# Optimization experiments

Measured on AMD Instinct MI355X. Metric: run time of the kernel, lower is better.

The kernel has to match this reference:

```python
import jax, jax.numpy as jnp
import numpy as np

B, C_IN, T = 32, 22, 5000
EMB, P = 64, 100
HOP, NFFT, SR = 25, 128, 250
MIN_SZ, MAX_SZ = 10, 100
OC = 40
SCALES = (9, 25, 49)
FC = OC * len(SCALES)
_freqs = np.arange(NFFT // 2 + 1) * SR / NFFT
MU_IDX = np.nonzero((_freqs >= 8) & (_freqs <= 13))[0]   # bins 5,6
BETA_IDX = np.nonzero((_freqs >= 13) & (_freqs <= 30))[0]  # bins 7..15


def setup_inputs() -> dict:
    key = jax.random.key(0)
    k = iter(jax.random.split(key, 16))
    inp = {"x": jax.random.normal(next(k), (B, C_IN, T), jnp.float32)}
    for i, s in enumerate(SCALES):
        inp[f"ms{i}_w1"] = jax.random.normal(next(k), (OC, 1, 1, s), jnp.float32) * 0.05
        inp[f"ms{i}_b1"] = jnp.zeros((OC,), jnp.float32)
        inp[f"ms{i}_w2"] = jax.random.normal(next(k), (OC, OC, C_IN, 1), jnp.float32) * 0.05
        inp[f"ms{i}_b2"] = jnp.zeros((OC,), jnp.float32)
        inp[f"ms{i}_g"] = jnp.ones((OC,), jnp.float32)
        inp[f"ms{i}_bt"] = jnp.zeros((OC,), jnp.float32)
        inp[f"ms{i}_m"] = jnp.zeros((OC,), jnp.float32)
        inp[f"ms{i}_v"] = jnp.ones((OC,), jnp.float32)
    inp["a_w1"] = jax.random.normal(next(k), (C_IN // 2, C_IN, 3), jnp.float32) * 0.05
    inp["a_b1"] = jnp.zeros((C_IN // 2,), jnp.float32)
    inp["a_g"] = jnp.ones((C_IN // 2,), jnp.float32)
    inp["a_bt"] = jnp.zeros((C_IN // 2,), jnp.float32)
    inp["a_m"] = jnp.zeros((C_IN // 2,), jnp.float32)
    inp["a_v"] = jnp.ones((C_IN // 2,), jnp.float32)
    inp["a_w2"] = jax.random.normal(next(k), (1, C_IN // 2, 1), jnp.float32) * 0.05
    inp["a_b2"] = jnp.zeros((1,), jnp.float32)
    inp["proj_w"] = jax.random.normal(next(k), (EMB, FC, 1), jnp.float32) * 0.05
    inp["proj_b"] = jnp.zeros((EMB,), jnp.float32)
    return inp


def _conv1d(x, w, pad):
    return jax.lax.conv_general_dilated(x, w, (1,), [(pad, pad)],
                                        dimension_numbers=("NCH", "OIH", "NCH"))


def _bn(y, g, bt, m, v):  # eval-mode BatchNorm over channel dim of [B, C, T]
    return (y - m[None, :, None]) * jax.lax.rsqrt(v[None, :, None] + 1e-5) * g[None, :, None] + bt[None, :, None]


def _branch(x, w1, b1, w2, b2, g, bt, m, v):
    # Conv2d(1,OC,(1,ks)) on [B,1,C,T] == per-channel 1D conv over time.
    oc, _, _, ks = w1.shape
    b_, c_, t_ = x.shape
    y = _conv1d(x.reshape(b_ * c_, 1, t_), w1.reshape(oc, 1, ks), (ks - 1) // 2) + b1[None, :, None]
    y = y.reshape(b_, c_, oc, t_).transpose(0, 2, 1, 3)            # [B, OC, C, T]
    # Conv2d(OC,OC,(C,1)) collapses the channel (height) dim.
    y = jnp.einsum("oih,biht->bot", w2[..., 0], y) + b2[None, :, None]
    return jax.nn.elu(_bn(y, g, bt, m, v))                         # [B, OC, T]


def _stft_power(x):
    # torchaudio Spectrogram: center=True, reflect pad, periodic hann, power=2
    pad = NFFT // 2
    xp = jnp.pad(x, ((0, 0), (0, 0), (pad, pad)), mode="reflect")
    nfr = T // HOP  # module truncates to t // hop frames
    idx = jnp.arange(nfr)[:, None] * HOP + jnp.arange(NFFT)[None, :]
    win = 0.5 * (1.0 - jnp.cos(2.0 * jnp.pi * jnp.arange(NFFT) / NFFT))
    frames = xp[..., idx] * win                                    # [B, C, nfr, NFFT]
    spec = jnp.fft.rfft(frames, axis=-1)
    return spec.real ** 2 + spec.imag ** 2                         # [B, C, nfr, NFFT//2+1]


def _interp_linear(a, n):  # F.interpolate(mode='linear', align_corners=False) on [B, L]
    L = a.shape[-1]
    pos = jnp.clip((jnp.arange(n) + 0.5) * (L / n) - 0.5, 0.0, L - 1.0)
    lo = jnp.floor(pos).astype(jnp.int32)
    hi = jnp.minimum(lo + 1, L - 1)
    w = pos - lo
    return a[:, lo] * (1.0 - w) + a[:, hi] * w


def _adaptive_grid(act):
    w = 1.0 / (act + 1e-6)
    w = w / jnp.sum(w, axis=1, keepdims=True)
    gs = jnp.clip(w * T, MIN_SZ, MAX_SZ)
    gs = gs * (T / jnp.sum(gs, axis=1, keepdims=True))
    gsr = jnp.round(gs).astype(jnp.int32)
    gsr = gsr.at[:, -1].add(T - jnp.sum(gsr, axis=1))
    gsf = jnp.clip(gsr, MIN_SZ, MAX_SZ)
    gsf = gsf.at[:, -1].add(T - jnp.sum(gsf, axis=1))
    return jnp.where(gsf < MIN_SZ, MIN_SZ, gsf)


def _forward(x, ms0_w1, ms0_b1, ms0_w2, ms0_b2, ms0_g, ms0_bt, ms0_m, ms0_v,
             ms1_w1, ms1_b1, ms1_w2, ms1_b2, ms1_g, ms1_bt, ms1_m, ms1_v,
             ms2_w1, ms2_b1, ms2_w2, ms2_b2, ms2_g, ms2_bt, ms2_m, ms2_v,
             a_w1, a_b1, a_g, a_bt, a_m, a_v, a_w2, a_b2, proj_w, proj_b):
    # ---- frequency-domain activity detector ----
    spec = _stft_power(x)                                          # [B, C, 200, F]
    comb = spec[..., MU_IDX].mean(-1) + spec[..., BETA_IDX].mean(-1)  # [B, C, 200]
    a = jax.nn.relu(_bn(_conv1d(comb, a_w1, 1) + a_b1[None, :, None], a_g, a_bt, a_m, a_v))
    a = jnp.einsum("oi,bit->bot", a_w2[..., 0], a)[:, 0] + a_b2[0]
    activity = jax.nn.sigmoid(a)                                   # [B, 200]
    act_i = _interp_linear(activity, P)                            # [B, P]
    grid = _adaptive_grid(act_i)                                   # [B, P] int32, sums ~= T
    ends = jnp.cumsum(grid, axis=1)
    starts = ends - grid
    # ---- multi-scale CNN features ----
    feats = jnp.concatenate([
        _branch(x, ms0_w1, ms0_b1, ms0_w2, ms0_b2, ms0_g, ms0_bt, ms0_m, ms0_v),
        _branch(x, ms1_w1, ms1_b1, ms1_w2, ms1_b2, ms1_g, ms1_bt, ms1_m, ms1_v),
        _branch(x, ms2_w1, ms2_b1, ms2_w2, ms2_b2, ms2_g, ms2_bt, ms2_m, ms2_v)],
        axis=1)                                                    # [B, FC, T]
    # ---- ragged per-patch avg+max pooling via segment reductions ----
    tix = jnp.arange(T)
    seg = jax.vmap(lambda e: jnp.searchsorted(e, tix, side="right"))(ends)  # [B,T] in [0,P]
    flat = (seg + jnp.arange(B)[:, None] * (P + 1)).reshape(-1)
    f = feats.transpose(0, 2, 1).reshape(B * T, FC)
    nseg = B * (P + 1)  # extra slot collects any overflow timesteps
    sums = jax.ops.segment_sum(f, flat, num_segments=nseg)
    cnt = jax.ops.segment_sum(jnp.ones((B * T, 1), f.dtype), flat, num_segments=nseg)
    mx = jax.ops.segment_max(f, flat, num_segments=nseg)
    avg = sums / jnp.maximum(cnt, 1.0)
    mx = jnp.where(cnt > 0, mx, 0.0)
    pooled = (avg + mx).reshape(B, P + 1, FC)[:, :P]               # combined avg+max
    valid = ((ends <= T) & (starts < ends))[..., None]
    pooled = jnp.where(valid, pooled, 0.0)
    emb = jnp.einsum("oc,bpc->bpo", proj_w[..., 0], pooled) + proj_b  # [B, P, EMB]
    return emb, grid, act_i


def reference(x, ms0_w1, ms0_b1, ms0_w2, ms0_b2, ms0_g, ms0_bt, ms0_m, ms0_v,
              ms1_w1, ms1_b1, ms1_w2, ms1_b2, ms1_g, ms1_bt, ms1_m, ms1_v,
              ms2_w1, ms2_b1, ms2_w2, ms2_b2, ms2_g, ms2_bt, ms2_m, ms2_v,
              a_w1, a_b1, a_g, a_bt, a_m, a_v, a_w2, a_b2, proj_w, proj_b):
    return _forward(x, ms0_w1, ms0_b1, ms0_w2, ms0_b2, ms0_g, ms0_bt, ms0_m, ms0_v,
                    ms1_w1, ms1_b1, ms1_w2, ms1_b2, ms1_g, ms1_bt, ms1_m, ms1_v,
                    ms2_w1, ms2_b1, ms2_w2, ms2_b2, ms2_g, ms2_bt, ms2_m, ms2_v,
                    a_w1, a_b1, a_g, a_bt, a_m, a_v, a_w2, a_b2, proj_w, proj_b)
```

## Files before the change

kernel.cpp:

```cpp
#include <hip/hip_runtime.h>
#include <hip/hip_bf16.h>
#include <math.h>
#include <string.h>

#define B 32
#define CIN 22
#define T 5000
#define EMB 64
#define P 100
#define HOP 25
#define OC 40
#define FC 120
#define NBIN 11
#define NFR 200

#define TCH 128
#define CROWS 176
#define RSTRIDE 40

#define XPAD 5128

typedef unsigned short ushort_t;
typedef __attribute__((ext_vector_type(8))) short bf16x8;
typedef __attribute__((ext_vector_type(4))) float f32x4;

__device__ __forceinline__ unsigned short f2bf(float f) {
  unsigned u = __float_as_uint(f);
  unsigned r = (u + 0x7FFFu + ((u >> 16) & 1u)) >> 16;
  return (unsigned short)r;
}
__device__ __forceinline__ float bf2f(unsigned short u) {
  return __uint_as_float(((unsigned)u) << 16);
}
__device__ __forceinline__ float fast_elu(float y) {
  return y > 0.f ? y : (__builtin_amdgcn_exp2f(y * 1.44269504088896340736f) - 1.0f);
}
__device__ __forceinline__ unsigned pack2bf(float a, float b) {
  __hip_bfloat162 h = __float22bfloat162_rn(make_float2(a, b));
  unsigned u;
  memcpy(&u, &h, 4);
  return u;
}

struct FrontArgs {
  const float* w1[3]; const float* b1[3]; const float* w2[3]; const float* b2[3];
  const float* g[3];  const float* bt[3]; const float* m[3];  const float* v[3];
  const float* x;
  unsigned short* pw;
  float* A; float* Bc; float* comb;
};

__global__ __launch_bounds__(256) void front_all(FrontArgs args) {
  __shared__ float fsm[XPAD + NBIN * 128 * 2];
  int bx = blockIdx.x;
  int tid = threadIdx.x;
  if (bx < 498) {
    int id = bx * 256 + tid;
    int s, KS, fbase, idl;
    if (id < 13824)       { s = 0; KS = 9;  fbase = 0;   idl = id; }
    else if (id < 52224)  { s = 1; KS = 25; fbase = 27;  idl = id - 13824; }
    else                  { s = 2; KS = 49; fbase = 102; idl = id - 52224; }
    int fi = idl >> 9, rem = idl & 511;
    int lane = rem >> 3, j = rem & 7;
    int k = fi / 3, ot = fi - k * 3;
    int m = lane & 15, h = ((lane >> 4) << 3) + j;
    int o = ot * 16 + m;
    float val = 0.f;
    if (h < CIN && o < OC) {
      const float* w1 = args.w1[s];
      const float* w2 = args.w2[s];
      for (int i = 0; i < OC; ++i)
        val = fmaf(w2[(o * OC + i) * CIN + h], w1[i * KS + k], val);
    }
    args.pw[(size_t)(fbase + fi) * 512 + rem] = f2bf(val);
  } else if (bx < 498 + B * CIN) {
    float* xsh = fsm;
    float* tw  = fsm + XPAD;
    int bc = bx - 498;
    const float* xr = args.x + (size_t)bc * T;
    const float TWO_PI_OVER_128 = 0.049087385212340517f;
    for (int i = tid; i < NBIN * 128; i += 256) {
      int k = i / 128 + 5, n = i - (i / 128) * 128;
      float ang = -TWO_PI_OVER_128 * (float)(k * n);
      float win = 0.5f * (1.0f - __cosf(TWO_PI_OVER_128 * (float)n));
      tw[2 * i]     = __cosf(ang) * win;
      tw[2 * i + 1] = __sinf(ang) * win;
    }
    for (int i = tid; i < XPAD; i += 256) {
      int mm = i - 64;
      mm = (mm < 0) ? -mm : mm;
      mm = (mm >= T) ? (2 * T - 2 - mm) : mm;
      xsh[i] = xr[mm];
    }
    __syncthreads();
    int fr = tid;
    if (fr < NFR) {
      float cr[NBIN], ci[NBIN];
      #pragma unroll
      for (int k = 0; k < NBIN; ++k) { cr[k] = 0.f; ci[k] = 0.f; }
      const float* xw = xsh + fr * HOP;
      for (int n = 0; n < 128; ++n) {
        float xv = xw[n];
        const float* twn = tw + 2 * n;
        #pragma unroll
        for (int k = 0; k < NBIN; ++k) {
          float2 w = *reinterpret_cast<const float2*>(twn + 256 * k);
          cr[k] = fmaf(xv, w.x, cr[k]);
          ci[k] = fmaf(xv, w.y, ci[k]);
        }
      }
      float p[NBIN];
      #pragma unroll
      for (int k = 0; k < NBIN; ++k) p[k] = cr[k] * cr[k] + ci[k] * ci[k];
      float beta = 0.f;
      #pragma unroll
      for (int k = 2; k < NBIN; ++k) beta += p[k];
      args.comb[bc * NFR + fr] = 0.5f * (p[0] + p[1]) + beta * (1.f / 9.f);
    }
  } else {
    if (tid < 120) {
      int s = tid / 40, o = tid - s * 40;
      const float* w2 = args.w2[s];
      float sc = args.g[s][o] / sqrtf(args.v[s][o] + 1e-5f);
      float cc = args.b2[s][o];
      for (int i = 0; i < OC; ++i) {
        float sh = 0.f;
        for (int h = 0; h < CIN; ++h) sh += w2[(o * OC + i) * CIN + h];
        cc = fmaf(args.b1[s][i], sh, cc);
      }
      args.A[tid] = sc;
      args.Bc[tid] = cc * sc + (args.bt[s][o] - args.m[s][o] * sc);
    }
  }
}

__device__ __forceinline__ float wave_sum_f(float v) {
  #pragma unroll
  for (int off = 1; off < 64; off <<= 1) v += __shfl_xor(v, off);
  return v;
}
__device__ __forceinline__ int wave_sum_i(int v) {
  #pragma unroll
  for (int off = 1; off < 64; off <<= 1) v += __shfl_xor(v, off);
  return v;
}

struct MidSmem {
  union {
    struct {
      float cl[CIN * NFR];
      float actL[NFR];
      float aiL[P];
      float fL[P];
      int giL[P];
      int sI[P];
      float red;
    } a;
    unsigned short xs[CROWS * RSTRIDE];
  };
};

template <int KS, int FB, int SBASE>
__device__ __forceinline__ void scale_body(const unsigned short* __restrict__ xs,
                                           const unsigned short* __restrict__ pw,
                                           const float* __restrict__ Aff,
                                           const float* __restrict__ Bff,
                                           unsigned short* __restrict__ feats,
                                           int b, int t0, int wt0, int lane) {
  constexpr int PAD = (KS - 1) / 2;
  const int n = lane & 15, q = lane >> 4;
  f32x4 acc[3][2];
  #pragma unroll
  for (int ot = 0; ot < 3; ++ot)
    #pragma unroll
    for (int ti = 0; ti < 2; ++ti)
      acc[ot][ti] = (f32x4){0.f, 0.f, 0.f, 0.f};

  const unsigned short* pws = pw + (size_t)FB * 512 + lane * 8;
  #pragma unroll 1
  for (int k = 0; k < KS; ++k) {
    bf16x8 A0 = *(const bf16x8*)(pws + (size_t)(k * 3 + 0) * 512);
    bf16x8 A1 = *(const bf16x8*)(pws + (size_t)(k * 3 + 1) * 512);
    bf16x8 A2 = *(const bf16x8*)(pws + (size_t)(k * 3 + 2) * 512);
    int rbase = 24 - PAD + k + wt0 + n;
    #pragma unroll
    for (int ti = 0; ti < 2; ++ti) {
      bf16x8 Bf = *(const bf16x8*)(xs + (rbase + ti * 16) * RSTRIDE + q * 8);
      acc[0][ti] = __builtin_amdgcn_mfma_f32_16x16x32_bf16(A0, Bf, acc[0][ti], 0, 0, 0);
      acc[1][ti] = __builtin_amdgcn_mfma_f32_16x16x32_bf16(A1, Bf, acc[1][ti], 0, 0, 0);
      acc[2][ti] = __builtin_amdgcn_mfma_f32_16x16x32_bf16(A2, Bf, acc[2][ti], 0, 0, 0);
    }
  }
  #pragma unroll
  for (int ot = 0; ot < 3; ++ot) {
    int obase = ot * 16 + q * 4;
    if (obase < OC) {
      float Av0 = Aff[SBASE + obase + 0], Bv0 = Bff[SBASE + obase + 0];
      float Av1 = Aff[SBASE + obase + 1], Bv1 = Bff[SBASE + obase + 1];
      float Av2 = Aff[SBASE + obase + 2], Bv2 = Bff[SBASE + obase + 2];
      float Av3 = Aff[SBASE + obase + 3], Bv3 = Bff[SBASE + obase + 3];
      #pragma unroll
      for (int ti = 0; ti < 2; ++ti) {
        int tt = t0 + wt0 + ti * 16 + n;
        if (tt < T) {
          uint2 pk;
          pk.x = pack2bf(fast_elu(fmaf(acc[ot][ti][0], Av0, Bv0)),
                         fast_elu(fmaf(acc[ot][ti][1], Av1, Bv1)));
          pk.y = pack2bf(fast_elu(fmaf(acc[ot][ti][2], Av2, Bv2)),
                         fast_elu(fmaf(acc[ot][ti][3], Av3, Bv3)));
          *reinterpret_cast<uint2*>(feats + (size_t)(b * T + tt) * FC + SBASE + obase) = pk;
        }
      }
    }
  }
}

struct MidArgs {
  const float* x;
  const unsigned short* pw;
  const float* Aff; const float* Bff;
  unsigned short* feats;
  const float* comb;
  const float* aw1; const float* ab1;
  const float* ag;  const float* abt;
  const float* am;  const float* av;
  const float* aw2; const float* ab2;
  float* out_grid; float* out_acti;
  int* ends_i; int* grid_i;
};

__global__ __launch_bounds__(256) void mid_all(MidArgs args) {
  __shared__ MidSmem sm;
  int bx = blockIdx.x;
  int tid = threadIdx.x;
  if (bx >= B) {
    int cx = bx - B;
    int b = cx / 40, t0 = (cx - b * 40) * TCH;
    for (int idx = tid; idx < CIN * CROWS; idx += 256) {
      int h = idx / CROWS, tl = idx - h * CROWS;
      int gt = t0 - 24 + tl;
      float v = (gt >= 0 && gt < T) ? args.x[(size_t)(b * CIN + h) * T + gt] : 0.f;
      sm.xs[tl * RSTRIDE + h] = f2bf(v);
    }
    for (int idx = tid; idx < 10 * CROWS; idx += 256) {
      int c = idx / CROWS, tl = idx - c * CROWS;
      sm.xs[tl * RSTRIDE + 22 + c] = 0;
    }
    __syncthreads();
    int wv = tid >> 6, lane = tid & 63;
    int wt0 = wv * 32;
    scale_body<9, 0, 0>(sm.xs, args.pw, args.Aff, args.Bff, args.feats, b, t0, wt0, lane);
    scale_body<25, 27, 40>(sm.xs, args.pw, args.Aff, args.Bff, args.feats, b, t0, wt0, lane);
    scale_body<49, 102, 80>(sm.xs, args.pw, args.Aff, args.Bff, args.feats, b, t0, wt0, lane);
  } else {
    int b = bx;
    for (int i = tid; i < CIN * NFR; i += 256) sm.a.cl[i] = args.comb[b * CIN * NFR + i];
    __syncthreads();
    int t = tid;
    if (t < NFR) {
      float z = args.ab2[0];
      for (int o = 0; o < 11; ++o) {
        float s = args.ab1[o];
        for (int i = 0; i < CIN; ++i) {
          const float* wr = args.aw1 + o * 66 + i * 3;
          const float* crow = sm.a.cl + i * NFR;
          if (t > 0)       s = fmaf(wr[0], crow[t - 1], s);
          s = fmaf(wr[1], crow[t], s);
          if (t < NFR - 1) s = fmaf(wr[2], crow[t + 1], s);
        }
        float rs = 1.0f / sqrtf(args.av[o] + 1e-5f);
        float y = (s - args.am[o]) * rs * args.ag[o] + args.abt[o];
        y = fmaxf(y, 0.f);
        z = fmaf(args.aw2[o], y, z);
      }
      sm.a.actL[t] = 1.f / (1.f + expf(-z));
    }
    __syncthreads();
    if (t < P) {
      float ai = 0.5f * (sm.a.actL[2 * t] + sm.a.actL[2 * t + 1]);
      sm.a.aiL[t] = ai;
      args.out_acti[b * P + t] = ai;
      sm.a.fL[t] = 1.f / (ai + 1e-6f);
    }
    __syncthreads();
    if (t < 64) {
      float v = sm.a.fL[t] + ((t + 64 < P) ? sm.a.fL[t + 64] : 0.f);
      v = wave_sum_f(v);
      if (t == 0) sm.a.red = v;
    }
    __syncthreads();
    float sw = sm.a.red;
    if (t < P) {
      float gg = (sm.a.fL[t] / sw) * 5000.f;
      gg = fminf(fmaxf(gg, 10.f), 100.f);
      sm.a.fL[t] = gg;
    }
    __syncthreads();
    if (t < 64) {
      float v = sm.a.fL[t] + ((t + 64 < P) ? sm.a.fL[t + 64] : 0.f);
      v = wave_sum_f(v);
      if (t == 0) sm.a.red = v;
    }
    __syncthreads();
    float r = 5000.f / sm.a.red;
    if (t < P) sm.a.giL[t] = (int)rintf(sm.a.fL[t] * r);
    __syncthreads();
    if (t < 64) {
      int v = sm.a.giL[t] + ((t + 64 < P) ? sm.a.giL[t + 64] : 0);
      v = wave_sum_i(v);
      if (t == 0) sm.a.red = __int_as_float(v);
    }
    __syncthreads();
    if (t == P - 1) sm.a.giL[P - 1] += 5000 - __float_as_int(sm.a.red);
    __syncthreads();
    if (t < P) sm.a.giL[t] = min(max(sm.a.giL[t], 10), 100);
    __syncthreads();
    if (t < 64) {
      int v = sm.a.giL[t] + ((t + 64 < P) ? sm.a.giL[t + 64] : 0);
      v = wave_sum_i(v);
      if (t == 0) sm.a.red = __int_as_float(v);
    }
    __syncthreads();
    if (t == P - 1) sm.a.giL[P - 1] += 5000 - __float_as_int(sm.a.red);
    __syncthreads();
    if (t < P) sm.a.sI[t] = max(sm.a.giL[t], 10);
    __syncthreads();
    #pragma unroll
    for (int off = 1; off < P; off <<= 1) {
      int v = 0;
      if (t < P && t >= off) v = sm.a.sI[t - off];
      __syncthreads();
      if (t < P) sm.a.sI[t] += v;
      __syncthreads();
    }
    if (t < P) {
      int g = max(sm.a.giL[t], 10);
      args.out_grid[b * P + t] = (float)g;
      args.grid_i[b * P + t] = g;
      args.ends_i[b * P + t] = sm.a.sI[t];
    }
  }
}

__global__ __launch_bounds__(256) void pool_proj(const unsigned short* __restrict__ feats,
                                                 const int* __restrict__ ends_i,
                                                 const int* __restrict__ grid_i,
                                                 const float* __restrict__ proj_w,
                                                 const float* __restrict__ proj_b,
                                                 float* __restrict__ out_emb) {
  int bp = blockIdx.x;
  int b = bp / P;
  int end = ends_i[bp];
  int gr = grid_i[bp];
  int start = end - gr;
  __shared__ float lds_s[16 * FC];
  __shared__ float lds_m[16 * FC];
  __shared__ float pooled[FC];
  int tid = threadIdx.x;
  bool valid = (end <= T);
  int g = tid % 15;
  int r = tid / 15;
  if (valid && r < 16) {
    float s[8], m[8];
    #pragma unroll
    for (int j = 0; j < 8; ++j) { s[j] = 0.f; m[j] = -INFINITY; }
    const unsigned short* base = feats + (size_t)(b * T + start) * FC + g * 8;
    for (int i = r; i < gr; i += 16) {
      uint4 u = *reinterpret_cast<const uint4*>(base + (size_t)i * FC);
      unsigned w[4] = {u.x, u.y, u.z, u.w};
      #pragma unroll
      for (int j = 0; j < 4; ++j) {
        float v0 = bf2f((unsigned short)(w[j] & 0xffffu));
        float v1 = bf2f((unsigned short)(w[j] >> 16));
        s[2 * j] += v0; s[2 * j + 1] += v1;
        m[2 * j] = fmaxf(m[2 * j], v0); m[2 * j + 1] = fmaxf(m[2 * j + 1], v1);
      }
    }
    #pragma unroll
    for (int j = 0; j < 8; ++j) {
      lds_s[r * FC + g * 8 + j] = s[j];
      lds_m[r * FC + g * 8 + j] = m[j];
    }
  }
  __syncthreads();
  if (tid < FC) {
    if (valid) {
      float s = 0.f, mx = -INFINITY;
      #pragma unroll
      for (int rr = 0; rr < 16; ++rr) {
        s += lds_s[rr * FC + tid];
        mx = fmaxf(mx, lds_m[rr * FC + tid]);
      }
      pooled[tid] = s / (float)gr + mx;
    } else {
      pooled[tid] = 0.f;
    }
  }
  __syncthreads();
  if (tid < EMB) {
    float e = proj_b[tid];
    const float* wr = proj_w + tid * FC;
    #pragma unroll 8
    for (int c = 0; c < FC; ++c) e = fmaf(wr[c], pooled[c], e);
    out_emb[(size_t)bp * EMB + tid] = e;
  }
}

extern "C" void kernel_launch(void* const* d_in, const int* in_sizes, int n_in,
                              void* d_out, int out_size, void* d_ws, size_t ws_size,
                              hipStream_t stream) {
  const float* x = (const float*)d_in[0];
  const float* aw1 = (const float*)d_in[25];
  const float* ab1 = (const float*)d_in[26];
  const float* ag  = (const float*)d_in[27];
  const float* abt = (const float*)d_in[28];
  const float* am  = (const float*)d_in[29];
  const float* av  = (const float*)d_in[30];
  const float* aw2 = (const float*)d_in[31];
  const float* ab2 = (const float*)d_in[32];
  const float* proj_w = (const float*)d_in[33];
  const float* proj_b = (const float*)d_in[34];

  float* wsf = (float*)d_ws;
  float* A    = wsf;
  float* Bc   = wsf + 120;
  float* comb = wsf + 3056;
  int* ends_i = (int*)(wsf + 143856);
  int* grid_i = (int*)(wsf + 147056);
  unsigned short* pw = (unsigned short*)(wsf + 150256);
  unsigned short* feats = (unsigned short*)(wsf + 214000);

  float* out      = (float*)d_out;
  float* out_emb  = out;
  float* out_grid = out + 204800;
  float* out_acti = out + 208000;

  FrontArgs fa;
  MidArgs ma;
  for (int s = 0; s < 3; ++s) {
    fa.w1[s] = (const float*)d_in[1 + 8 * s];
    fa.b1[s] = (const float*)d_in[2 + 8 * s];
    fa.w2[s] = (const float*)d_in[3 + 8 * s];
    fa.b2[s] = (const float*)d_in[4 + 8 * s];
    fa.g[s]  = (const float*)d_in[5 + 8 * s];
    fa.bt[s] = (const float*)d_in[6 + 8 * s];
    fa.m[s]  = (const float*)d_in[7 + 8 * s];
    fa.v[s]  = (const float*)d_in[8 + 8 * s];
  }
  fa.x = x; fa.pw = pw; fa.A = A; fa.Bc = Bc; fa.comb = comb;

  ma.x = x; ma.pw = pw; ma.Aff = A; ma.Bff = Bc; ma.feats = feats;
  ma.comb = comb; ma.aw1 = aw1; ma.ab1 = ab1; ma.ag = ag; ma.abt = abt;
  ma.am = am; ma.av = av; ma.aw2 = aw2; ma.ab2 = ab2;
  ma.out_grid = out_grid; ma.out_acti = out_acti;
  ma.ends_i = ends_i; ma.grid_i = grid_i;

  front_all<<<498 + B * CIN + 1, 256, 0, stream>>>(fa);
  mid_all<<<B + 40 * B, 256, 0, stream>>>(ma);
  pool_proj<<<B * P, 256, 0, stream>>>(feats, ends_i, grid_i, proj_w, proj_b, out_emb);
}
```

Before: 260.3 us.

## Split STFT into separate kernel with global twiddle table and widen conv time tiles

```diff
diff --git a/kernel.cpp b/kernel.cpp
--- a/kernel.cpp
+++ b/kernel.cpp
@@ -14,11 +14,12 @@
 #define NBIN 11
 #define NFR 200
 
-#define TCH 128
-#define CROWS 176
+#define TCH 256
+#define CROWS 304
 #define RSTRIDE 40
 
 #define XPAD 5128
+#define TWROW 24
 
 typedef unsigned short ushort_t;
 typedef __attribute__((ext_vector_type(8))) short bf16x8;
@@ -42,16 +43,14 @@
   return u;
 }
 
-struct FrontArgs {
+struct SetupArgs {
   const float* w1[3]; const float* b1[3]; const float* w2[3]; const float* b2[3];
   const float* g[3];  const float* bt[3]; const float* m[3];  const float* v[3];
-  const float* x;
   unsigned short* pw;
-  float* A; float* Bc; float* comb;
+  float* A; float* Bc; float* tw;
 };
 
-__global__ __launch_bounds__(256) void front_all(FrontArgs args) {
-  __shared__ float fsm[XPAD + NBIN * 128 * 2];
+__global__ __launch_bounds__(256) void setup_all(SetupArgs args) {
   int bx = blockIdx.x;
   int tid = threadIdx.x;
   if (bx < 498) {
@@ -73,49 +72,19 @@
         val = fmaf(w2[(o * OC + i) * CIN + h], w1[i * KS + k], val);
     }
     args.pw[(size_t)(fbase + fi) * 512 + rem] = f2bf(val);
-  } else if (bx < 498 + B * CIN) {
-    float* xsh = fsm;
-    float* tw  = fsm + XPAD;
-    int bc = bx - 498;
-    const float* xr = args.x + (size_t)bc * T;
-    const float TWO_PI_OVER_128 = 0.049087385212340517f;
-    for (int i = tid; i < NBIN * 128; i += 256) {
-      int k = i / 128 + 5, n = i - (i / 128) * 128;
-      float ang = -TWO_PI_OVER_128 * (float)(k * n);
-      float win = 0.5f * (1.0f - __cosf(TWO_PI_OVER_128 * (float)n));
-      tw[2 * i]     = __cosf(ang) * win;
-      tw[2 * i + 1] = __sinf(ang) * win;
-    }
-    for (int i = tid; i < XPAD; i += 256) {
-      int mm = i - 64;
-      mm = (mm < 0) ? -mm : mm;
-      mm = (mm >= T) ? (2 * T - 2 - mm) : mm;
-      xsh[i] = xr[mm];
-    }
-    __syncthreads();
-    int fr = tid;
-    if (fr < NFR) {
-      float cr[NBIN], ci[NBIN];
-      #pragma unroll
-      for (int k = 0; k < NBIN; ++k) { cr[k] = 0.f; ci[k] = 0.f; }
-      const float* xw = xsh + fr * HOP;
-      for (int n = 0; n < 128; ++n) {
-        float xv = xw[n];
-        const float* twn = tw + 2 * n;
-        #pragma unroll
-        for (int k = 0; k < NBIN; ++k) {
-          float2 w = *reinterpret_cast<const float2*>(twn + 256 * k);
-          cr[k] = fmaf(xv, w.x, cr[k]);
-          ci[k] = fmaf(xv, w.y, ci[k]);
-        }
-      }
-      float p[NBIN];
-      #pragma unroll
-      for (int k = 0; k < NBIN; ++k) p[k] = cr[k] * cr[k] + ci[k] * ci[k];
-      float beta = 0.f;
-      #pragma unroll
-      for (int k = 2; k < NBIN; ++k) beta += p[k];
-      args.comb[bc * NFR + fr] = 0.5f * (p[0] + p[1]) + beta * (1.f / 9.f);
+  } else if (bx < 504) {
+    int id = (bx - 498) * 256 + tid;
+    if (id < 1408) {
+      int n = id & 127, k = id >> 7;
+      const double PI = 3.14159265358979323846;
+      double ang = -2.0 * PI * (double)((k + 5) * n) / 128.0;
+      double win = 0.5 * (1.0 - cos(2.0 * PI * (double)n / 128.0));
+      args.tw[n * TWROW + 2 * k]     = (float)(cos(ang) * win);
+      args.tw[n * TWROW + 2 * k + 1] = (float)(sin(ang) * win);
+    } else if (id < 1536) {
+      int n = id - 1408;
+      args.tw[n * TWROW + 22] = 0.f;
+      args.tw[n * TWROW + 23] = 0.f;
     }
   } else {
     if (tid < 120) {
@@ -131,6 +100,53 @@
       args.A[tid] = sc;
       args.Bc[tid] = cc * sc + (args.bt[s][o] - args.m[s][o] * sc);
     }
+  }
+}
+
+__global__ __launch_bounds__(256) void stft_comb(const float* __restrict__ x,
+                                                 const float* __restrict__ tw,
+                                                 float* __restrict__ comb) {
+  __shared__ float xsh[XPAD];
+  int bc = blockIdx.x;
+  const float* xr = x + (size_t)bc * T;
+  int tid = threadIdx.x;
+  for (int i = tid; i < XPAD; i += 256) {
+    int mm = i - 64;
+    mm = (mm < 0) ? -mm : mm;
+    mm = (mm >= T) ? (2 * T - 2 - mm) : mm;
+    xsh[i] = xr[mm];
+  }
+  __syncthreads();
+  int fr = tid;
+  if (fr < NFR) {
+    float cr[NBIN], ci[NBIN];
+    #pragma unroll
+    for (int k = 0; k < NBIN; ++k) { cr[k] = 0.f; ci[k] = 0.f; }
+    const float* xw = xsh + fr * HOP;
+    #pragma unroll 2
+    for (int n = 0; n < 128; ++n) {
+      float xv = xw[n];
+      const float4* t4 = reinterpret_cast<const float4*>(tw + n * TWROW);
+      float4 w0 = t4[0], w1 = t4[1], w2 = t4[2], w3 = t4[3], w4 = t4[4], w5 = t4[5];
+      cr[0] = fmaf(xv, w0.x, cr[0]); ci[0] = fmaf(xv, w0.y, ci[0]);
+      cr[1] = fmaf(xv, w0.z, cr[1]); ci[1] = fmaf(xv, w0.w, ci[1]);
+      cr[2] = fmaf(xv, w1.x, cr[2]); ci[2] = fmaf(xv, w1.y, ci[2]);
+      cr[3] = fmaf(xv, w1.z, cr[3]); ci[3] = fmaf(xv, w1.w, ci[3]);
+      cr[4] = fmaf(xv, w2.x, cr[4]); ci[4] = fmaf(xv, w2.y, ci[4]);
+      cr[5] = fmaf(xv, w2.z, cr[5]); ci[5] = fmaf(xv, w2.w, ci[5]);
+      cr[6] = fmaf(xv, w3.x, cr[6]); ci[6] = fmaf(xv, w3.y, ci[6]);
+      cr[7] = fmaf(xv, w3.z, cr[7]); ci[7] = fmaf(xv, w3.w, ci[7]);
+      cr[8] = fmaf(xv, w4.x, cr[8]); ci[8] = fmaf(xv, w4.y, ci[8]);
+      cr[9] = fmaf(xv, w4.z, cr[9]); ci[9] = fmaf(xv, w4.w, ci[9]);
+      cr[10] = fmaf(xv, w5.x, cr[10]); ci[10] = fmaf(xv, w5.y, ci[10]);
+    }
+    float p[NBIN];
+    #pragma unroll
+    for (int k = 0; k < NBIN; ++k) p[k] = cr[k] * cr[k] + ci[k] * ci[k];
+    float beta = 0.f;
+    #pragma unroll
+    for (int k = 2; k < NBIN; ++k) beta += p[k];
+    comb[bc * NFR + fr] = 0.5f * (p[0] + p[1]) + beta * (1.f / 9.f);
   }
 }
 
@@ -169,11 +185,11 @@
                                            int b, int t0, int wt0, int lane) {
   constexpr int PAD = (KS - 1) / 2;
   const int n = lane & 15, q = lane >> 4;
-  f32x4 acc[3][2];
+  f32x4 acc[3][4];
   #pragma unroll
   for (int ot = 0; ot < 3; ++ot)
     #pragma unroll
-    for (int ti = 0; ti < 2; ++ti)
+    for (int ti = 0; ti < 4; ++ti)
       acc[ot][ti] = (f32x4){0.f, 0.f, 0.f, 0.f};
 
   const unsigned short* pws = pw + (size_t)FB * 512 + lane * 8;
@@ -184,7 +200,7 @@
     bf16x8 A2 = *(const bf16x8*)(pws + (size_t)(k * 3 + 2) * 512);
     int rbase = 24 - PAD + k + wt0 + n;
     #pragma unroll
-    for (int ti = 0; ti < 2; ++ti) {
+    for (int ti = 0; ti < 4; ++ti) {
       bf16x8 Bf = *(const bf16x8*)(xs + (rbase + ti * 16) * RSTRIDE + q * 8);
       acc[0][ti] = __builtin_amdgcn_mfma_f32_16x16x32_bf16(A0, Bf, acc[0][ti], 0, 0, 0);
       acc[1][ti] = __builtin_amdgcn_mfma_f32_16x16x32_bf16(A1, Bf, acc[1][ti], 0, 0, 0);
@@ -200,7 +216,7 @@
       float Av2 = Aff[SBASE + obase + 2], Bv2 = Bff[SBASE + obase + 2];
       float Av3 = Aff[SBASE + obase + 3], Bv3 = Bff[SBASE + obase + 3];
       #pragma unroll
-      for (int ti = 0; ti < 2; ++ti) {
+      for (int ti = 0; ti < 4; ++ti) {
         int tt = t0 + wt0 + ti * 16 + n;
         if (tt < T) {
           uint2 pk;
@@ -235,7 +251,7 @@
   int tid = threadIdx.x;
   if (bx >= B) {
     int cx = bx - B;
-    int b = cx / 40, t0 = (cx - b * 40) * TCH;
+    int b = cx / 20, t0 = (cx - b * 20) * TCH;
     for (int idx = tid; idx < CIN * CROWS; idx += 256) {
       int h = idx / CROWS, tl = idx - h * CROWS;
       int gt = t0 - 24 + tl;
@@ -248,7 +264,7 @@
     }
     __syncthreads();
     int wv = tid >> 6, lane = tid & 63;
-    int wt0 = wv * 32;
+    int wt0 = wv * 64;
     scale_body<9, 0, 0>(sm.xs, args.pw, args.Aff, args.Bff, args.feats, b, t0, wt0, lane);
     scale_body<25, 27, 40>(sm.xs, args.pw, args.Aff, args.Bff, args.feats, b, t0, wt0, lane);
     scale_body<49, 102, 80>(sm.xs, args.pw, args.Aff, args.Bff, args.feats, b, t0, wt0, lane);
@@ -424,30 +440,31 @@
   float* wsf = (float*)d_ws;
   float* A    = wsf;
   float* Bc   = wsf + 120;
-  float* comb = wsf + 3056;
-  int* ends_i = (int*)(wsf + 143856);
-  int* grid_i = (int*)(wsf + 147056);
-  unsigned short* pw = (unsigned short*)(wsf + 150256);
-  unsigned short* feats = (unsigned short*)(wsf + 214000);
+  float* tw   = wsf + 240;
+  float* comb = wsf + 4096;
+  int* ends_i = (int*)(wsf + 144896);
+  int* grid_i = (int*)(wsf + 148096);
+  unsigned short* pw = (unsigned short*)(wsf + 151296);
+  unsigned short* feats = (unsigned short*)(wsf + 215040);
 
   float* out      = (float*)d_out;
   float* out_emb  = out;
   float* out_grid = out + 204800;
   float* out_acti = out + 208000;
 
-  FrontArgs fa;
+  SetupArgs sa;
   MidArgs ma;
   for (int s = 0; s < 3; ++s) {
-    fa.w1[s] = (const float*)d_in[1 + 8 * s];
-    fa.b1[s] = (const float*)d_in[2 + 8 * s];
-    fa.w2[s] = (const float*)d_in[3 + 8 * s];
-    fa.b2[s] = (const float*)d_in[4 + 8 * s];
-    fa.g[s]  = (const float*)d_in[5 + 8 * s];
-    fa.bt[s] = (const float*)d_in[6 + 8 * s];
-    fa.m[s]  = (const float*)d_in[7 + 8 * s];
-    fa.v[s]  = (const float*)d_in[8 + 8 * s];
-  }
-  fa.x = x; fa.pw = pw; fa.A = A; fa.Bc = Bc; fa.comb = comb;
+    sa.w1[s] = (const float*)d_in[1 + 8 * s];
+    sa.b1[s] = (const float*)d_in[2 + 8 * s];
+    sa.w2[s] = (const float*)d_in[3 + 8 * s];
+    sa.b2[s] = (const float*)d_in[4 + 8 * s];
+    sa.g[s]  = (const float*)d_in[5 + 8 * s];
+    sa.bt[s] = (const float*)d_in[6 + 8 * s];
+    sa.m[s]  = (const float*)d_in[7 + 8 * s];
+    sa.v[s]  = (const float*)d_in[8 + 8 * s];
+  }
+  sa.pw = pw; sa.A = A; sa.Bc = Bc; sa.tw = tw;
 
   ma.x = x; ma.pw = pw; ma.Aff = A; ma.Bff = Bc; ma.feats = feats;
   ma.comb = comb; ma.aw1 = aw1; ma.ab1 = ab1; ma.ag = ag; ma.abt = abt;
@@ -455,7 +472,8 @@
   ma.out_grid = out_grid; ma.out_acti = out_acti;
   ma.ends_i = ends_i; ma.grid_i = grid_i;
 
-  front_all<<<498 + B * CIN + 1, 256, 0, stream>>>(fa);
-  mid_all<<<B + 40 * B, 256, 0, stream>>>(ma);
+  setup_all<<<505, 256, 0, stream>>>(sa);
+  stft_comb<<<B * CIN, 256, 0, stream>>>(x, tw, comb);
+  mid_all<<<B + 20 * B, 256, 0, stream>>>(ma);
   pool_proj<<<B * P, 256, 0, stream>>>(feats, ends_i, grid_i, proj_w, proj_b, out_emb);
 }
```

After: 262.8 us. No clear change (+1.0%).
